# Performance work log

Measured on AMD Instinct MI355X. Metric: run time of the kernel, lower is better.

The kernel has to match this reference:

```python
import jax, jax.numpy as jnp
import numpy as np

N = 100000      # nodes
E = 3200000     # edges (avg degree 32)
F_IN = 256      # n_features
HID = 128       # n_hidden
C = 16          # n_classes
K = 10          # propagation hops


def setup_inputs() -> dict:
    key = jax.random.key(0)
    ks = jax.random.split(key, 12)
    x = jax.random.normal(ks[0], (N, F_IN), jnp.float32)
    edge_index = jax.random.randint(ks[1], (2, E), 0, N, dtype=jnp.int64)
    edge_attr = jax.random.uniform(ks[2], (E,), jnp.float32)
    # learned parameters (torch Linear layout: W [out, in], b [out])
    def lin(k, fan_out, fan_in):
        s = 1.0 / np.sqrt(fan_in)
        kw, kb = jax.random.split(k)
        W = jax.random.uniform(kw, (fan_out, fan_in), jnp.float32, -s, s)
        b = jax.random.uniform(kb, (fan_out,), jnp.float32, -s, s)
        return W, b
    lin1_w, lin1_b = lin(ks[3], HID, F_IN)
    lin2_w, lin2_b = lin(ks[4], HID, HID)   # hidden lin (n_layers-3 == 1)
    lin3_w, lin3_b = lin(ks[5], C, HID)     # classes lin
    proj_w, proj_b = lin(ks[6], 1, C)       # Prop retain-score projection
    return {"x": x, "edge_index": edge_index, "edge_attr": edge_attr,
            "lin1_w": lin1_w, "lin1_b": lin1_b,
            "lin2_w": lin2_w, "lin2_b": lin2_b,
            "lin3_w": lin3_w, "lin3_b": lin3_b,
            "proj_w": proj_w, "proj_b": proj_b}


def reference(x, edge_index, edge_attr,
              lin1_w, lin1_b, lin2_w, lin2_b, lin3_w, lin3_b,
              proj_w, proj_b):
    # MLP stack (dropout is identity in eval mode)
    h = jax.nn.relu(x @ lin1_w.T + lin1_b)
    h = jax.nn.relu(h @ lin2_w.T + lin2_b)
    h = jax.nn.relu(h @ lin3_w.T + lin3_b)          # [N, C]

    src, dst = edge_index[0], edge_index[1]
    norm = edge_attr[:, None]                        # [E, 1]

    def hop(carry, _):
        msg = norm * carry[src]                      # gather + scale [E, C]
        nxt = jax.ops.segment_sum(msg, dst, num_segments=N)  # scatter-add
        return nxt, nxt

    _, hops = jax.lax.scan(hop, h, None, length=K)   # [K, N, C]
    pps = jnp.concatenate([h[None], hops], axis=0)   # [K+1, N, C]
    pps = jnp.transpose(pps, (1, 0, 2))              # [N, K+1, C]

    # adaptive combination: sigmoid(Linear(C->1)) per hop, weighted sum
    score = jax.nn.sigmoid(jnp.einsum('nkc,c->nk', pps, proj_w[0]) + proj_b[0])
    out = jnp.einsum('nk,nkc->nc', score, pps)       # [N, C]
    return out
```

## Files before the change

### kernel.cpp

```cpp
#include <hip/hip_runtime.h>
#include <hip/hip_bf16.h>
#include <math.h>

#define N_NODES 100000
#define E_EDGES 3200000
#define K_HOPS  10
#define NPP     256
#define NPART   ((N_NODES + NPP - 1) / NPP)
#define CHUNK   4096
#define EPT     (CHUNK / 256)
#define NCHUNK  ((E_EDGES + CHUNK - 1) / CHUNK)
#define NFLAT   (NPART * NCHUNK)
#define SSEG    8192
#define GA      ((NFLAT + SSEG - 1) / SSEG)

typedef __attribute__((ext_vector_type(8))) short short8;
typedef __attribute__((ext_vector_type(4))) float floatx4;

__device__ __forceinline__ ushort f2bf(float f) {
    uint u = __float_as_uint(f);
    u += 0x7fffu + ((u >> 16) & 1u);
    return (ushort)(u >> 16);
}
__device__ __forceinline__ uint pk2(float a, float b) {
    return (uint)f2bf(a) | ((uint)f2bf(b) << 16);
}
__device__ __forceinline__ float bflo(uint u) { return __uint_as_float(u << 16); }
__device__ __forceinline__ float bfhi(uint u) { return __uint_as_float(u & 0xffff0000u); }

__global__ __launch_bounds__(256, 2) void fused_mlp(
    const float* __restrict__ X,
    const float* __restrict__ W1, const float* __restrict__ B1,
    const float* __restrict__ W2, const float* __restrict__ B2,
    const float* __restrict__ W3, const float* __restrict__ B3,
    const float* __restrict__ PW, const float* __restrict__ PB,
    ushort* __restrict__ H0,
    float* __restrict__ OUT)
{
    __shared__ ushort Wl[128 * 64];
    __shared__ ushort Hb[128 * 128];

    const int t    = threadIdx.x;
    const int w    = t >> 6;
    const int lane = t & 63;
    const int m    = lane & 15;
    const int quad = lane >> 4;
    const int rowBase = blockIdx.x * 128 + w * 32;
    const int swm = (m & 7) << 3;

    short8 afr[2][8];
#pragma unroll
    for (int rt = 0; rt < 2; ++rt) {
        int row = rowBase + rt * 16 + m;
        row = row < N_NODES ? row : N_NODES - 1;
        const float* xp = X + (size_t)row * 256 + quad * 8;
#pragma unroll
        for (int kk = 0; kk < 8; ++kk) {
            floatx4 a0 = *(const floatx4*)(xp + kk * 32);
            floatx4 a1 = *(const floatx4*)(xp + kk * 32 + 4);
            short8 v;
            v[0] = (short)f2bf(a0[0]); v[1] = (short)f2bf(a0[1]);
            v[2] = (short)f2bf(a0[2]); v[3] = (short)f2bf(a0[3]);
            v[4] = (short)f2bf(a1[0]); v[5] = (short)f2bf(a1[1]);
            v[6] = (short)f2bf(a1[2]); v[7] = (short)f2bf(a1[3]);
            afr[rt][kk] = v;
        }
    }

    floatx4 acc[2][8];
#pragma unroll
    for (int rt = 0; rt < 2; ++rt)
#pragma unroll
        for (int ct = 0; ct < 8; ++ct) acc[rt][ct] = (floatx4)0.f;

#pragma unroll
    for (int kb4 = 0; kb4 < 4; ++kb4) {
#pragma unroll
        for (int j = 0; j < 8; ++j) {
            int flat = j * 256 + t;
            int n  = flat >> 4;
            int c4 = (flat & 15) * 4;
            floatx4 v = *(const floatx4*)&W1[(size_t)n * 256 + kb4 * 64 + c4];
            *(uint2*)&Wl[n * 64 + (c4 ^ ((n & 7) << 3))] =
                make_uint2(pk2(v[0], v[1]), pk2(v[2], v[3]));
        }
        __syncthreads();
#pragma unroll
        for (int ks = 0; ks < 2; ++ks) {
#pragma unroll
            for (int ct = 0; ct < 8; ++ct) {
                short8 bf = *(const short8*)
                    &Wl[(ct * 16 + m) * 64 + ((ks * 32 + quad * 8) ^ swm)];
                acc[0][ct] = __builtin_amdgcn_mfma_f32_16x16x32_bf16(
                    afr[0][kb4 * 2 + ks], bf, acc[0][ct], 0, 0, 0);
                acc[1][ct] = __builtin_amdgcn_mfma_f32_16x16x32_bf16(
                    afr[1][kb4 * 2 + ks], bf, acc[1][ct], 0, 0, 0);
            }
        }
        __syncthreads();
    }

    {
        float br[8];
#pragma unroll
        for (int ct = 0; ct < 8; ++ct) br[ct] = B1[ct * 16 + m];
#pragma unroll
        for (int rt = 0; rt < 2; ++rt)
#pragma unroll
            for (int r = 0; r < 4; ++r) {
                int lrow = w * 32 + rt * 16 + quad * 4 + r;
                int sw = (lrow & 7) << 3;
#pragma unroll
                for (int ct = 0; ct < 8; ++ct) {
                    float v = acc[rt][ct][r] + br[ct];
                    v = v > 0.f ? v : 0.f;
                    Hb[lrow * 128 + ((ct * 16 + m) ^ sw)] = f2bf(v);
                }
            }
    }

#pragma unroll
    for (int rt = 0; rt < 2; ++rt)
#pragma unroll
        for (int ct = 0; ct < 8; ++ct) acc[rt][ct] = (floatx4)0.f;

#pragma unroll
    for (int kb2 = 0; kb2 < 2; ++kb2) {
#pragma unroll
        for (int j = 0; j < 8; ++j) {
            int flat = j * 256 + t;
            int n  = flat >> 4;
            int c4 = (flat & 15) * 4;
            floatx4 v = *(const floatx4*)&W2[(size_t)n * 128 + kb2 * 64 + c4];
            *(uint2*)&Wl[n * 64 + (c4 ^ ((n & 7) << 3))] =
                make_uint2(pk2(v[0], v[1]), pk2(v[2], v[3]));
        }
        __syncthreads();
#pragma unroll
        for (int ks = 0; ks < 2; ++ks) {
            short8 af[2];
#pragma unroll
            for (int rt = 0; rt < 2; ++rt) {
                int lrow = w * 32 + rt * 16 + m;
                int col  = kb2 * 64 + ks * 32 + quad * 8;
                af[rt] = *(const short8*)&Hb[lrow * 128 + (col ^ swm)];
            }
#pragma unroll
            for (int ct = 0; ct < 8; ++ct) {
                short8 bf = *(const short8*)
                    &Wl[(ct * 16 + m) * 64 + ((ks * 32 + quad * 8) ^ swm)];
                acc[0][ct] = __builtin_amdgcn_mfma_f32_16x16x32_bf16(
                    af[0], bf, acc[0][ct], 0, 0, 0);
                acc[1][ct] = __builtin_amdgcn_mfma_f32_16x16x32_bf16(
                    af[1], bf, acc[1][ct], 0, 0, 0);
            }
        }
        __syncthreads();
    }

    {
        float br[8];
#pragma unroll
        for (int ct = 0; ct < 8; ++ct) br[ct] = B2[ct * 16 + m];
#pragma unroll
        for (int rt = 0; rt < 2; ++rt)
#pragma unroll
            for (int r = 0; r < 4; ++r) {
                int lrow = w * 32 + rt * 16 + quad * 4 + r;
                int sw = (lrow & 7) << 3;
#pragma unroll
                for (int ct = 0; ct < 8; ++ct) {
                    float v = acc[rt][ct][r] + br[ct];
                    v = v > 0.f ? v : 0.f;
                    Hb[lrow * 128 + ((ct * 16 + m) ^ sw)] = f2bf(v);
                }
            }
    }

#pragma unroll
    for (int j = 0; j < 2; ++j) {
        int flat = j * 256 + t;
        int n  = flat >> 5;
        int c4 = (flat & 31) * 4;
        floatx4 v = *(const floatx4*)&W3[(size_t)n * 128 + c4];
        *(uint2*)&Wl[n * 128 + (c4 ^ ((n & 7) << 3))] =
            make_uint2(pk2(v[0], v[1]), pk2(v[2], v[3]));
    }
    __syncthreads();

    floatx4 acc3[2];
    acc3[0] = (floatx4)0.f; acc3[1] = (floatx4)0.f;
#pragma unroll
    for (int ks4 = 0; ks4 < 4; ++ks4) {
        int col = ks4 * 32 + quad * 8;
        short8 bf = *(const short8*)&Wl[m * 128 + (col ^ swm)];
#pragma unroll
        for (int rt = 0; rt < 2; ++rt) {
            int lrow = w * 32 + rt * 16 + m;
            short8 af = *(const short8*)&Hb[lrow * 128 + (col ^ swm)];
            acc3[rt] = __builtin_amdgcn_mfma_f32_16x16x32_bf16(
                af, bf, acc3[rt], 0, 0, 0);
        }
    }

    const float pwm = PW[m];
    const float b3m = B3[m];
    const float pb0 = PB[0];
#pragma unroll
    for (int rt = 0; rt < 2; ++rt)
#pragma unroll
        for (int r = 0; r < 4; ++r) {
            int row = rowBase + rt * 16 + quad * 4 + r;
            float v = acc3[rt][r] + b3m;
            v = v > 0.f ? v : 0.f;
            float part = v * pwm;
            part += __shfl_xor(part, 1);
            part += __shfl_xor(part, 2);
            part += __shfl_xor(part, 4);
            part += __shfl_xor(part, 8);
            float s = 1.f / (1.f + __expf(-(part + pb0)));
            if (row < N_NODES) {
                OUT[(size_t)row * 16 + m] = s * v;
                H0[(size_t)row * 16 + m]  = f2bf(v);
            }
        }
}

__global__ __launch_bounds__(256) void hist2(
    const int* __restrict__ dst, int* __restrict__ cmat)
{
    __shared__ int lhist[NPART];
    const int t = threadIdx.x;
    for (int p = t; p < NPART; p += 256) lhist[p] = 0;
    __syncthreads();
    const int base = blockIdx.x * CHUNK;
#pragma unroll
    for (int j = 0; j < EPT; ++j) {
        int i = base + j * 256 + t;
        if (i < E_EDGES) atomicAdd(&lhist[dst[i] >> 8], 1);
    }
    __syncthreads();
    for (int p = t; p < NPART; p += 256)
        cmat[p * NCHUNK + blockIdx.x] = lhist[p];
}

__global__ __launch_bounds__(1024) void scan_reduce(
    const int* __restrict__ cmat, int* __restrict__ bsum)
{
    __shared__ int wsum[16];
    const int t = threadIdx.x, lane = t & 63, wid = t >> 6;
    int base = blockIdx.x * SSEG + t * 8;
    int s = 0;
#pragma unroll
    for (int j = 0; j < 8; ++j) {
        int idx = base + j;
        if (idx < NFLAT) s += cmat[idx];
    }
#pragma unroll
    for (int d = 1; d < 64; d <<= 1) s += __shfl_xor(s, d);
    if (lane == 0) wsum[wid] = s;
    __syncthreads();
    if (t == 0) {
        int tot = 0;
#pragma unroll
        for (int i = 0; i < 16; ++i) tot += wsum[i];
        bsum[blockIdx.x] = tot;
    }
}

__global__ void scan_tops(const int* __restrict__ bsum, int* __restrict__ boff)
{
    const int t = threadIdx.x;
    int v = (t < GA) ? bsum[t] : 0;
    int x = v;
#pragma unroll
    for (int d = 1; d < 64; d <<= 1) {
        int y = __shfl_up(x, d);
        if (t >= d) x += y;
    }
    if (t < GA) boff[t] = x - v;
}

__global__ __launch_bounds__(1024) void scan_apply(
    int* __restrict__ cmat, const int* __restrict__ boff, int* __restrict__ pbase)
{
    __shared__ int wsum[16];
    __shared__ int woff[17];
    const int t = threadIdx.x, lane = t & 63, wid = t >> 6;
    int base = blockIdx.x * SSEG + t * 8;
    int v[8], pre[8];
    int s = 0;
#pragma unroll
    for (int j = 0; j < 8; ++j) {
        int idx = base + j;
        v[j] = (idx < NFLAT) ? cmat[idx] : 0;
        pre[j] = s;
        s += v[j];
    }
    int x = s;
#pragma unroll
    for (int d = 1; d < 64; d <<= 1) {
        int y = __shfl_up(x, d);
        if (lane >= d) x += y;
    }
    if (lane == 63) wsum[wid] = x;
    __syncthreads();
    if (wid == 0) {
        int w = (lane < 16) ? wsum[lane] : 0;
#pragma unroll
        for (int d = 1; d < 16; d <<= 1) {
            int y = __shfl_up(w, d);
            if (lane >= d) w += y;
        }
        if (lane < 16) woff[lane + 1] = w;
        if (lane == 0) woff[0] = 0;
    }
    __syncthreads();
    int tbase = boff[blockIdx.x] + woff[wid] + (x - s);
#pragma unroll
    for (int j = 0; j < 8; ++j) {
        int idx = base + j;
        if (idx < NFLAT) {
            int e = tbase + pre[j];
            cmat[idx] = e;
            if (idx % NCHUNK == 0) pbase[idx / NCHUNK] = e;
        }
    }
    if (blockIdx.x == 0 && t == 0) pbase[NPART] = E_EDGES;
}

__global__ __launch_bounds__(256) void scatter3(
    const int* __restrict__ src, const int* __restrict__ dst,
    const float* __restrict__ ea, const int* __restrict__ cbase,
    int2* __restrict__ staging)
{
    __shared__ int2 ebuf[CHUNK];
    __shared__ int  gaddr[CHUNK];
    __shared__ int  lcnt[NPART];
    __shared__ int  goff[NPART];
    __shared__ int  wsum[4];
    const int t = threadIdx.x;
    const int b = blockIdx.x;
    const int base = b * CHUNK;
    const int cnt = min(CHUNK, E_EDGES - base);
    const int lane = t & 63, wid = t >> 6;

    for (int p = t; p < NPART; p += 256) lcnt[p] = 0;
    __syncthreads();

    int d[EPT];
#pragma unroll
    for (int j = 0; j < EPT; ++j) {
        int i = base + j * 256 + t;
        d[j] = (i < E_EDGES) ? dst[i] : -1;
        if (d[j] >= 0) atomicAdd(&lcnt[d[j] >> 8], 1);
    }
    __syncthreads();

    int v0 = (2 * t     < NPART) ? lcnt[2 * t]     : 0;
    int v1 = (2 * t + 1 < NPART) ? lcnt[2 * t + 1] : 0;
    int pair = v0 + v1;
    int x = pair;
#pragma unroll
    for (int dd = 1; dd < 64; dd <<= 1) {
        int y = __shfl_up(x, dd);
        if (lane >= dd) x += y;
    }
    if (lane == 63) wsum[wid] = x;
    __syncthreads();
    int wbase = 0;
#pragma unroll
    for (int w = 0; w < 4; ++w) if (w < wid) wbase += wsum[w];
    int excl = wbase + x - pair;
    if (2 * t < NPART) {
        lcnt[2 * t] = excl;
        goff[2 * t] = cbase[(2 * t) * NCHUNK + b] - excl;
    }
    if (2 * t + 1 < NPART) {
        lcnt[2 * t + 1] = excl + v0;
        goff[2 * t + 1] = cbase[(2 * t + 1) * NCHUNK + b] - (excl + v0);
    }
    __syncthreads();

#pragma unroll
    for (int j = 0; j < EPT; ++j) {
        if (d[j] >= 0) {
            int i = base + j * 256 + t;
            int p = d[j] >> 8;
            int s = atomicAdd(&lcnt[p], 1);
            ebuf[s]  = make_int2(__float_as_int(ea[i]),
                                 src[i] | ((d[j] & 255) << 17));
            gaddr[s] = goff[p] + s;
        }
    }
    __syncthreads();

    for (int k = t; k < cnt; k += 256)
        staging[gaddr[k]] = ebuf[k];
}

__global__ __launch_bounds__(1024) void partition_build(
    const int2* __restrict__ staging, const int* __restrict__ pbase,
    int* __restrict__ rowp, int2* __restrict__ csr)
{
    __shared__ int ncnt[NPP];
    __shared__ int wsum[4];
    const int p = blockIdx.x;
    const int t = threadIdx.x;
    const int e0 = pbase[p], e1 = pbase[p + 1];
    const int cnt = e1 - e0;
    const int n0 = p << 8;

    if (t < NPP) ncnt[t] = 0;
    __syncthreads();
    for (int e = t; e < cnt; e += 1024)
        atomicAdd(&ncnt[(staging[e0 + e].y >> 17) & 255], 1);
    __syncthreads();

    int x = 0, v = 0;
    if (t < NPP) {
        const int lane = t & 63, wid = t >> 6;
        v = ncnt[t];
        x = v;
#pragma unroll
        for (int d = 1; d < 64; d <<= 1) {
            int y = __shfl_up(x, d);
            if (lane >= d) x += y;
        }
        if (lane == 63) wsum[wid] = x;
    }
    __syncthreads();
    if (t < NPP) {
        const int wid = t >> 6;
        int wbase = 0;
#pragma unroll
        for (int w = 0; w < 4; ++w) if (w < wid) wbase += wsum[w];
        int excl = wbase + x - v;
        ncnt[t] = e0 + excl;
        int n = n0 + t;
        if (n < N_NODES) rowp[n] = e0 + excl;
    }
    if (p == NPART - 1 && t == 0) rowp[N_NODES] = E_EDGES;
    __syncthreads();

    for (int e = t; e < cnt; e += 1024) {
        int2 en = staging[e0 + e];
        int dlo = (en.y >> 17) & 255;
        int pos = atomicAdd(&ncnt[dlo], 1);
        csr[pos] = make_int2(en.y & 0x1FFFF, en.x);
    }
}

__global__ __launch_bounds__(256) void hop_bf16(
    const ushort* __restrict__ prev, ushort* __restrict__ next,
    const int* __restrict__ rowp, const int2* __restrict__ csr,
    const float* __restrict__ pw, const float* __restrict__ pb,
    float* __restrict__ out)
{
    const int t = threadIdx.x;
    const int l = t & 1;
    const int g = (t >> 1) & 3;
    const int n = blockIdx.x * 32 + (t >> 3);
    if (n >= N_NODES) return;
    const int e0 = rowp[n], e1 = rowp[n + 1];
    float a[8];
#pragma unroll
    for (int j = 0; j < 8; ++j) a[j] = 0.f;

    int e = e0 + g;
    for (; e + 12 < e1; e += 16) {
        int2 c0 = csr[e];
        int2 c1 = csr[e + 4];
        int2 c2 = csr[e + 8];
        int2 c3 = csr[e + 12];
        float w0 = __int_as_float(c0.y), w1 = __int_as_float(c1.y);
        float w2 = __int_as_float(c2.y), w3 = __int_as_float(c3.y);
        uint4 v0 = *(const uint4*)&prev[(size_t)c0.x * 16 + l * 8];
        uint4 v1 = *(const uint4*)&prev[(size_t)c1.x * 16 + l * 8];
        uint4 v2 = *(const uint4*)&prev[(size_t)c2.x * 16 + l * 8];
        uint4 v3 = *(const uint4*)&prev[(size_t)c3.x * 16 + l * 8];
        a[0] += w0 * bflo(v0.x); a[1] += w0 * bfhi(v0.x);
        a[2] += w0 * bflo(v0.y); a[3] += w0 * bfhi(v0.y);
        a[4] += w0 * bflo(v0.z); a[5] += w0 * bfhi(v0.z);
        a[6] += w0 * bflo(v0.w); a[7] += w0 * bfhi(v0.w);
        a[0] += w1 * bflo(v1.x); a[1] += w1 * bfhi(v1.x);
        a[2] += w1 * bflo(v1.y); a[3] += w1 * bfhi(v1.y);
        a[4] += w1 * bflo(v1.z); a[5] += w1 * bfhi(v1.z);
        a[6] += w1 * bflo(v1.w); a[7] += w1 * bfhi(v1.w);
        a[0] += w2 * bflo(v2.x); a[1] += w2 * bfhi(v2.x);
        a[2] += w2 * bflo(v2.y); a[3] += w2 * bfhi(v2.y);
        a[4] += w2 * bflo(v2.z); a[5] += w2 * bfhi(v2.z);
        a[6] += w2 * bflo(v2.w); a[7] += w2 * bfhi(v2.w);
        a[0] += w3 * bflo(v3.x); a[1] += w3 * bfhi(v3.x);
        a[2] += w3 * bflo(v3.y); a[3] += w3 * bfhi(v3.y);
        a[4] += w3 * bflo(v3.z); a[5] += w3 * bfhi(v3.z);
        a[6] += w3 * bflo(v3.w); a[7] += w3 * bfhi(v3.w);
    }
    for (; e < e1; e += 4) {
        int2 c0 = csr[e];
        float w0 = __int_as_float(c0.y);
        uint4 v0 = *(const uint4*)&prev[(size_t)c0.x * 16 + l * 8];
        a[0] += w0 * bflo(v0.x); a[1] += w0 * bfhi(v0.x);
        a[2] += w0 * bflo(v0.y); a[3] += w0 * bfhi(v0.y);
        a[4] += w0 * bflo(v0.z); a[5] += w0 * bfhi(v0.z);
        a[6] += w0 * bflo(v0.w); a[7] += w0 * bfhi(v0.w);
    }

#pragma unroll
    for (int d = 2; d <= 4; d <<= 1) {
#pragma unroll
        for (int j = 0; j < 8; ++j) a[j] += __shfl_xor(a[j], d);
    }

    float4 p0 = ((const float4*)pw)[l * 2];
    float4 p1 = ((const float4*)pw)[l * 2 + 1];
    float part = a[0]*p0.x + a[1]*p0.y + a[2]*p0.z + a[3]*p0.w
               + a[4]*p1.x + a[5]*p1.y + a[6]*p1.z + a[7]*p1.w;
    part += __shfl_xor(part, 1);
    float s = 1.f / (1.f + __expf(-(part + pb[0])));

    if (g == 0) {
        uint4 nv = make_uint4(pk2(a[0], a[1]), pk2(a[2], a[3]),
                              pk2(a[4], a[5]), pk2(a[6], a[7]));
        *(uint4*)&next[(size_t)n * 16 + l * 8] = nv;
        float4 o0 = *(float4*)&out[(size_t)n * 16 + l * 8];
        float4 o1 = *(float4*)&out[(size_t)n * 16 + l * 8 + 4];
        o0.x += s*a[0]; o0.y += s*a[1]; o0.z += s*a[2]; o0.w += s*a[3];
        o1.x += s*a[4]; o1.y += s*a[5]; o1.z += s*a[6]; o1.w += s*a[7];
        *(float4*)&out[(size_t)n * 16 + l * 8]     = o0;
        *(float4*)&out[(size_t)n * 16 + l * 8 + 4] = o1;
    }
}

extern "C" void kernel_launch(void* const* d_in, const int* in_sizes, int n_in,
                              void* d_out, int out_size, void* d_ws, size_t ws_size,
                              hipStream_t stream)
{
    const float* x  = (const float*)d_in[0];
    const int*   ei = (const int*)d_in[1];
    const float* ea = (const float*)d_in[2];
    const float* w1 = (const float*)d_in[3];
    const float* b1 = (const float*)d_in[4];
    const float* w2 = (const float*)d_in[5];
    const float* b2 = (const float*)d_in[6];
    const float* w3 = (const float*)d_in[7];
    const float* b3 = (const float*)d_in[8];
    const float* pw = (const float*)d_in[9];
    const float* pb = (const float*)d_in[10];
    float* out = (float*)d_out;

    char* ws = (char*)d_ws;
    size_t off = 0;
    char*   region0 = ws + off;           off += (size_t)E_EDGES * 16;
    ushort* pingb = (ushort*)(ws + off);  off += (size_t)N_NODES * 16 * 2;
    ushort* pongb = (ushort*)(ws + off);  off += (size_t)N_NODES * 16 * 2;
    int*    rowp  = (int*)(ws + off);     off += (((size_t)(N_NODES + 1) * 4) + 15) & ~(size_t)15;
    int*    cmat  = (int*)(ws + off);     off += ((size_t)NFLAT * 4 + 15) & ~(size_t)15;
    int*    bsum  = (int*)(ws + off);     off += ((size_t)GA * 4 + 15) & ~(size_t)15;
    int*    boff  = (int*)(ws + off);     off += ((size_t)GA * 4 + 15) & ~(size_t)15;
    int*    pbase = (int*)(ws + off);     off += ((size_t)(NPART + 1) * 4 + 15) & ~(size_t)15;
    int2*   csr   = (int2*)(ws + off);    off += (size_t)E_EDGES * 8;

    int2*   staging = (int2*)region0;

    const int* src = ei;
    const int* dst = ei + E_EDGES;

    const dim3 blk(256);
    const int mlpGrid    = (N_NODES + 127) / 128;
    const int hopGrid    = (N_NODES + 31) / 32;

    hist2<<<NCHUNK, blk, 0, stream>>>(dst, cmat);
    scan_reduce<<<GA, 1024, 0, stream>>>(cmat, bsum);
    scan_tops<<<1, 64, 0, stream>>>(bsum, boff);
    scan_apply<<<GA, 1024, 0, stream>>>(cmat, boff, pbase);
    scatter3<<<NCHUNK, blk, 0, stream>>>(src, dst, ea, cmat, staging);
    partition_build<<<NPART, 1024, 0, stream>>>(staging, pbase, rowp, csr);

    fused_mlp<<<mlpGrid, blk, 0, stream>>>(x, w1, b1, w2, b2, w3, b3,
                                           pw, pb, pingb, out);

    const ushort* prev = pingb;
    ushort* next = pongb;
    for (int k = 0; k < K_HOPS; ++k) {
        hop_bf16<<<hopGrid, blk, 0, stream>>>(prev, next, rowp, csr, pw, pb, out);
        ushort* tmp = (ushort*)prev; prev = next; next = tmp;
    }
}
```

Measured before the change: 577.2 us.

## Defer adaptive hop combination into single final kernel over stored hops

Each hop's bf16 result is now kept in a per-hop buffer that reuses the staging region, instead of ping-pong buffers. The sigmoid-scored accumulation into the output is removed from the MLP and hop kernels and done once at the end by a new combine kernel. This removes the per-hop read-modify-write of the fp32 output, which is 6.4 MB each hop. In exchange the combine kernel must re-read all 11 hop buffers at the end, and it adds one extra launch.

```diff
diff --git a/kernel.cpp b/kernel.cpp
--- a/kernel.cpp
+++ b/kernel.cpp
@@ -33,9 +33,7 @@
     const float* __restrict__ W1, const float* __restrict__ B1,
     const float* __restrict__ W2, const float* __restrict__ B2,
     const float* __restrict__ W3, const float* __restrict__ B3,
-    const float* __restrict__ PW, const float* __restrict__ PB,
-    ushort* __restrict__ H0,
-    float* __restrict__ OUT)
+    ushort* __restrict__ H0)
 {
     __shared__ ushort Wl[128 * 64];
     __shared__ ushort Hb[128 * 128];
@@ -203,9 +201,7 @@
         }
     }
 
-    const float pwm = PW[m];
     const float b3m = B3[m];
-    const float pb0 = PB[0];
 #pragma unroll
     for (int rt = 0; rt < 2; ++rt)
 #pragma unroll
@@ -213,16 +209,7 @@
             int row = rowBase + rt * 16 + quad * 4 + r;
             float v = acc3[rt][r] + b3m;
             v = v > 0.f ? v : 0.f;
-            float part = v * pwm;
-            part += __shfl_xor(part, 1);
-            part += __shfl_xor(part, 2);
-            part += __shfl_xor(part, 4);
-            part += __shfl_xor(part, 8);
-            float s = 1.f / (1.f + __expf(-(part + pb0)));
-            if (row < N_NODES) {
-                OUT[(size_t)row * 16 + m] = s * v;
-                H0[(size_t)row * 16 + m]  = f2bf(v);
-            }
+            if (row < N_NODES) H0[(size_t)row * 16 + m] = f2bf(v);
         }
 }
 
@@ -453,9 +440,7 @@
 
 __global__ __launch_bounds__(256) void hop_bf16(
     const ushort* __restrict__ prev, ushort* __restrict__ next,
-    const int* __restrict__ rowp, const int2* __restrict__ csr,
-    const float* __restrict__ pw, const float* __restrict__ pb,
-    float* __restrict__ out)
+    const int* __restrict__ rowp, const int2* __restrict__ csr)
 {
     const int t = threadIdx.x;
     const int l = t & 1;
@@ -512,24 +497,42 @@
         for (int j = 0; j < 8; ++j) a[j] += __shfl_xor(a[j], d);
     }
 
-    float4 p0 = ((const float4*)pw)[l * 2];
-    float4 p1 = ((const float4*)pw)[l * 2 + 1];
-    float part = a[0]*p0.x + a[1]*p0.y + a[2]*p0.z + a[3]*p0.w
-               + a[4]*p1.x + a[5]*p1.y + a[6]*p1.z + a[7]*p1.w;
-    part += __shfl_xor(part, 1);
-    float s = 1.f / (1.f + __expf(-(part + pb[0])));
-
     if (g == 0) {
         uint4 nv = make_uint4(pk2(a[0], a[1]), pk2(a[2], a[3]),
                               pk2(a[4], a[5]), pk2(a[6], a[7]));
         *(uint4*)&next[(size_t)n * 16 + l * 8] = nv;
-        float4 o0 = *(float4*)&out[(size_t)n * 16 + l * 8];
-        float4 o1 = *(float4*)&out[(size_t)n * 16 + l * 8 + 4];
-        o0.x += s*a[0]; o0.y += s*a[1]; o0.z += s*a[2]; o0.w += s*a[3];
-        o1.x += s*a[4]; o1.y += s*a[5]; o1.z += s*a[6]; o1.w += s*a[7];
-        *(float4*)&out[(size_t)n * 16 + l * 8]     = o0;
-        *(float4*)&out[(size_t)n * 16 + l * 8 + 4] = o1;
-    }
+    }
+}
+
+__global__ __launch_bounds__(256) void combine_all(
+    const ushort* __restrict__ hops,
+    const float* __restrict__ pw, const float* __restrict__ pb,
+    float* __restrict__ out)
+{
+    const int t = threadIdx.x;
+    const int l = t & 1;
+    const int n = blockIdx.x * 128 + (t >> 1);
+    if (n >= N_NODES) return;
+    float4 p0 = ((const float4*)pw)[l * 2];
+    float4 p1 = ((const float4*)pw)[l * 2 + 1];
+    const float pb0 = pb[0];
+    float o0 = 0.f, o1 = 0.f, o2 = 0.f, o3 = 0.f;
+    float o4 = 0.f, o5 = 0.f, o6 = 0.f, o7 = 0.f;
+#pragma unroll
+    for (int k = 0; k <= K_HOPS; ++k) {
+        uint4 v = *(const uint4*)
+            &hops[((size_t)k * N_NODES + n) * 16 + l * 8];
+        float a0 = bflo(v.x), a1 = bfhi(v.x), a2 = bflo(v.y), a3 = bfhi(v.y);
+        float a4 = bflo(v.z), a5 = bfhi(v.z), a6 = bflo(v.w), a7 = bfhi(v.w);
+        float part = a0*p0.x + a1*p0.y + a2*p0.z + a3*p0.w
+                   + a4*p1.x + a5*p1.y + a6*p1.z + a7*p1.w;
+        part += __shfl_xor(part, 1);
+        float s = 1.f / (1.f + __expf(-(part + pb0)));
+        o0 += s*a0; o1 += s*a1; o2 += s*a2; o3 += s*a3;
+        o4 += s*a4; o5 += s*a5; o6 += s*a6; o7 += s*a7;
+    }
+    *(float4*)&out[(size_t)n * 16 + l * 8]     = make_float4(o0, o1, o2, o3);
+    *(float4*)&out[(size_t)n * 16 + l * 8 + 4] = make_float4(o4, o5, o6, o7);
 }
 
 extern "C" void kernel_launch(void* const* d_in, const int* in_sizes, int n_in,
@@ -552,8 +555,6 @@
     char* ws = (char*)d_ws;
     size_t off = 0;
     char*   region0 = ws + off;           off += (size_t)E_EDGES * 16;
-    ushort* pingb = (ushort*)(ws + off);  off += (size_t)N_NODES * 16 * 2;
-    ushort* pongb = (ushort*)(ws + off);  off += (size_t)N_NODES * 16 * 2;
     int*    rowp  = (int*)(ws + off);     off += (((size_t)(N_NODES + 1) * 4) + 15) & ~(size_t)15;
     int*    cmat  = (int*)(ws + off);     off += ((size_t)NFLAT * 4 + 15) & ~(size_t)15;
     int*    bsum  = (int*)(ws + off);     off += ((size_t)GA * 4 + 15) & ~(size_t)15;
@@ -562,6 +563,8 @@
     int2*   csr   = (int2*)(ws + off);    off += (size_t)E_EDGES * 8;
 
     int2*   staging = (int2*)region0;
+    ushort* hops    = (ushort*)region0;
+    const size_t HSTRIDE = (size_t)N_NODES * 16;
 
     const int* src = ei;
     const int* dst = ei + E_EDGES;
@@ -577,13 +580,13 @@
     scatter3<<<NCHUNK, blk, 0, stream>>>(src, dst, ea, cmat, staging);
     partition_build<<<NPART, 1024, 0, stream>>>(staging, pbase, rowp, csr);
 
-    fused_mlp<<<mlpGrid, blk, 0, stream>>>(x, w1, b1, w2, b2, w3, b3,
-                                           pw, pb, pingb, out);
-
-    const ushort* prev = pingb;
-    ushort* next = pongb;
+    fused_mlp<<<mlpGrid, blk, 0, stream>>>(x, w1, b1, w2, b2, w3, b3, hops);
+
     for (int k = 0; k < K_HOPS; ++k) {
-        hop_bf16<<<hopGrid, blk, 0, stream>>>(prev, next, rowp, csr, pw, pb, out);
-        ushort* tmp = (ushort*)prev; prev = next; next = tmp;
-    }
-}
+        hop_bf16<<<hopGrid, blk, 0, stream>>>(hops + (size_t)k * HSTRIDE,
+                                              hops + (size_t)(k + 1) * HSTRIDE,
+                                              rowp, csr);
+    }
+
+    combine_all<<<mlpGrid, blk, 0, stream>>>(hops, pw, pb, out);
+}
```

Result: faster. 560.0 us, median of 2 (-3.0%).
